# Optimization experiments

Hardware: AMD Instinct MI355X
Metric: run time of the kernel (lower is better)

## Reference

```python
import jax, jax.numpy as jnp
import numpy as np

N = 100000
E = 1600000
IN_DIM = 128
HID = 64
HEADS = 1
NEG_SLOPE = 0.2


def setup_inputs() -> dict:
    key = jax.random.key(0)
    ks = jax.random.split(key, 12)
    x = jax.random.normal(ks[0], (N, IN_DIM), dtype=jnp.float32)
    edge_index = jax.random.randint(ks[1], (2, E), 0, N, dtype=jnp.int64)
    s1 = 1.0 / np.sqrt(IN_DIM)
    s2 = 1.0 / np.sqrt(HEADS * HID)
    return {
        "x": x,
        "edge_index": edge_index,
        # layer 1: in_dim -> heads*hid
        "W1": jax.random.normal(ks[2], (IN_DIM, HEADS * HID), dtype=jnp.float32) * s1,
        "a_src1": jax.random.normal(ks[3], (HEADS, HID), dtype=jnp.float32) * s1,
        "a_dst1": jax.random.normal(ks[4], (HEADS, HID), dtype=jnp.float32) * s1,
        "b1": jnp.zeros((HEADS * HID,), dtype=jnp.float32),
        # layer 2: heads*hid -> hid (1 head)
        "W2": jax.random.normal(ks[5], (HEADS * HID, HID), dtype=jnp.float32) * s2,
        "a_src2": jax.random.normal(ks[6], (1, HID), dtype=jnp.float32) * s2,
        "a_dst2": jax.random.normal(ks[7], (1, HID), dtype=jnp.float32) * s2,
        "b2": jnp.zeros((HID,), dtype=jnp.float32),
        # output head
        "W_out": jax.random.normal(ks[8], (HID, 1), dtype=jnp.float32) * (1.0 / np.sqrt(HID)),
        "b_out": jnp.zeros((1,), dtype=jnp.float32),
    }


def _gat_conv(x, src, dst, W, a_src, a_dst, bias, heads, hid):
    n = x.shape[0]
    h = (x @ W).reshape(n, heads, hid)                      # [N, H, D]
    alpha_s = jnp.einsum("nhd,hd->nh", h, a_src)            # [N, H]
    alpha_d = jnp.einsum("nhd,hd->nh", h, a_dst)
    e = alpha_s[src] + alpha_d[dst]                          # [E, H]
    e = jax.nn.leaky_relu(e, NEG_SLOPE)
    # segment softmax over edges sharing the same destination node
    m = jax.ops.segment_max(e, dst, num_segments=n)          # [N, H]
    ex = jnp.exp(e - m[dst])
    denom = jax.ops.segment_sum(ex, dst, num_segments=n)     # [N, H]
    alpha = ex / denom[dst]                                  # [E, H]
    out = jax.ops.segment_sum(h[src] * alpha[:, :, None], dst, num_segments=n)
    return out.reshape(n, heads * hid) + bias


def reference(x, edge_index, W1, a_src1, a_dst1, b1, W2, a_src2, a_dst2, b2, W_out, b_out):
    n = x.shape[0]
    # PyG GATConv default add_self_loops=True
    loops = jnp.arange(n, dtype=edge_index.dtype)
    src = jnp.concatenate([edge_index[0], loops])
    dst = jnp.concatenate([edge_index[1], loops])
    h = jax.nn.elu(_gat_conv(x, src, dst, W1, a_src1, a_dst1, b1, HEADS, HID))
    h = jax.nn.elu(_gat_conv(h, src, dst, W2, a_src2, a_dst2, b2, 1, HID))
    return (h @ W_out + b_out).squeeze(-1)                   # [N]
```

## Files before the change

kernel.cpp:

```cpp
#include <hip/hip_runtime.h>
#include <hip/hip_fp16.h>
#include <math.h>

#define NEG_SLOPE 0.2f
#define BKT_SHIFT 8
#define BKT_NODES (1 << BKT_SHIFT)
#define BKT_CAP 512
#define BKT_FCAP 6144
#define BKT_SHARD (BKT_FCAP / 4)
#define P1_CHUNK 4096

typedef _Float16 f16x8 __attribute__((ext_vector_type(8)));
typedef float    f32x4 __attribute__((ext_vector_type(4)));
union FU  { uint4 u; f16x8 f; };
union H2U { __half2 h; unsigned u; };

__device__ __forceinline__ float lrelu(float x){ return fmaxf(x, NEG_SLOPE * x); }
__device__ __forceinline__ float elu_fast(float x){
  float t = __expf(fminf(x, 0.f)) - 1.f;
  return x > 0.f ? x : t;
}


__global__ __launch_bounds__(256) void k_p1(const int* __restrict__ src, const int* __restrict__ dst,
                                            int E, int B, int* __restrict__ bktCur,
                                            unsigned* __restrict__ pairs,
                                            const float* __restrict__ W1, const float* __restrict__ W2,
                                            uint4* __restrict__ W1f, uint4* __restrict__ W2f){
  __shared__ int h[BKT_CAP], base[BKT_CAP], cur[BKT_CAP];
  int tid = threadIdx.x;
  if (blockIdx.x == 0){
    for (int idx = tid; idx < 16 * 64; idx += 256){
      int lane = idx & 63, fs = idx >> 6;
      int t = fs >> 2, s = fs & 3;
      int m = lane & 15, quad = lane >> 4;
      f16x8 v;
      #pragma unroll
      for (int j = 0; j < 8; ++j)
        v[j] = (_Float16)W1[(s * 32 + quad * 8 + j) * 64 + t * 16 + m];
      FU fu; fu.f = v;
      W1f[fs * 64 + lane] = fu.u;
    }
    for (int idx = tid; idx < 8 * 64; idx += 256){
      int lane = idx & 63, fs = idx >> 6;
      int t = fs >> 1, s = fs & 1;
      int m = lane & 15, quad = lane >> 4;
      f16x8 v;
      #pragma unroll
      for (int j = 0; j < 8; ++j)
        v[j] = (_Float16)W2[(s * 32 + quad * 8 + j) * 64 + t * 16 + m];
      FU fu; fu.f = v;
      W2f[fs * 64 + lane] = fu.u;
    }
  }
  for (int i = tid; i < BKT_CAP; i += 256){ h[i] = 0; cur[i] = 0; }
  __syncthreads();
  int beg = blockIdx.x * P1_CHUNK;
  int end = min(beg + P1_CHUNK, E);
  int shard = blockIdx.x & 3;
  int m4 = (end - beg) >> 2;
  const int4* d4 = (const int4*)(dst + beg);
  const int4* s4 = (const int4*)(src + beg);
  for (int i = tid; i < m4; i += 256){
    int4 d = d4[i];
    atomicAdd(&h[d.x >> BKT_SHIFT], 1); atomicAdd(&h[d.y >> BKT_SHIFT], 1);
    atomicAdd(&h[d.z >> BKT_SHIFT], 1); atomicAdd(&h[d.w >> BKT_SHIFT], 1);
  }
  for (int i = beg + (m4 << 2) + tid; i < end; i += 256)
    atomicAdd(&h[dst[i] >> BKT_SHIFT], 1);
  __syncthreads();
  for (int i = tid; i < B; i += 256)
    if (h[i]) base[i] = i * BKT_FCAP + shard * BKT_SHARD + atomicAdd(&bktCur[i * 4 + shard], h[i]);
  __syncthreads();
  for (int i = tid; i < m4; i += 256){
    int4 d = d4[i]; int4 s = s4[i];
    int b0 = d.x >> BKT_SHIFT, b1 = d.y >> BKT_SHIFT, b2 = d.z >> BKT_SHIFT, b3 = d.w >> BKT_SHIFT;
    int p0 = base[b0] + atomicAdd(&cur[b0], 1);
    pairs[p0] = ((unsigned)(d.x & (BKT_NODES-1)) << 17) | (unsigned)s.x;
    int p1 = base[b1] + atomicAdd(&cur[b1], 1);
    pairs[p1] = ((unsigned)(d.y & (BKT_NODES-1)) << 17) | (unsigned)s.y;
    int p2 = base[b2] + atomicAdd(&cur[b2], 1);
    pairs[p2] = ((unsigned)(d.z & (BKT_NODES-1)) << 17) | (unsigned)s.z;
    int p3 = base[b3] + atomicAdd(&cur[b3], 1);
    pairs[p3] = ((unsigned)(d.w & (BKT_NODES-1)) << 17) | (unsigned)s.w;
  }
  for (int i = beg + (m4 << 2) + tid; i < end; i += 256){
    int d = dst[i], s = src[i];
    int b = d >> BKT_SHIFT;
    int p = base[b] + atomicAdd(&cur[b], 1);
    pairs[p] = ((unsigned)(d & (BKT_NODES-1)) << 17) | (unsigned)s;
  }
}

__global__ __launch_bounds__(256) void k_p2(const unsigned* __restrict__ pairs,
                                            const int* __restrict__ bktCur,
                                            int N, int2* __restrict__ offs2, int* __restrict__ col){
  __shared__ int sc[BKT_NODES], cu[BKT_NODES];
  int b = blockIdx.x, tid = threadIdx.x;
  int nbase = b << BKT_SHIFT;
  int bs = b * BKT_FCAP;
  sc[tid] = 0;
  __syncthreads();
  #pragma unroll
  for (int s = 0; s < 4; ++s){
    int ss_ = bs + s * BKT_SHARD;
    int se_ = ss_ + bktCur[b * 4 + s];
    for (int i = ss_ + tid; i < se_; i += 256)
      atomicAdd(&sc[pairs[i] >> 17], 1);
  }
  __syncthreads();
  int v = sc[tid];
  for (int o = 1; o < 256; o <<= 1){
    int x = (tid >= o) ? sc[tid - o] : 0;
    __syncthreads();
    sc[tid] += x;
    __syncthreads();
  }
  int ex = sc[tid] - v;
  cu[tid] = bs + ex;
  if (nbase + tid < N) offs2[nbase + tid] = make_int2(bs + ex, bs + ex + v);
  __syncthreads();
  #pragma unroll
  for (int s = 0; s < 4; ++s){
    int ss_ = bs + s * BKT_SHARD;
    int se_ = ss_ + bktCur[b * 4 + s];
    for (int i = ss_ + tid; i < se_; i += 256){
      unsigned pr = pairs[i];
      int p = atomicAdd(&cu[pr >> 17], 1);
      col[p] = (int)(pr & 0x1FFFFu);
    }
  }
}

__global__ __launch_bounds__(256) void k_mgemm1(
    const float* __restrict__ X, const uint4* __restrict__ Wf,
    const float* __restrict__ a_src, const float* __restrict__ a_dst,
    uint2* __restrict__ H, float* __restrict__ as_, float* __restrict__ ad_, int n)
{
  int lane = threadIdx.x & 63, wv = threadIdx.x >> 6;
  int quad = lane >> 4, nn = lane & 15;
  int rowb = blockIdx.x * 64 + wv * 16;
  int row = rowb + nn;
  bool ok = row < n;
  int rowc = ok ? row : n - 1;

  f16x8 af[4][4];
  #pragma unroll
  for (int t = 0; t < 4; ++t)
    #pragma unroll
    for (int s = 0; s < 4; ++s){
      FU fu; fu.u = Wf[(t * 4 + s) * 64 + lane];
      af[t][s] = fu.f;
    }

  const float4* Xr = (const float4*)(X + (size_t)rowc * 128);
  float4 xb[4][2];
  #pragma unroll
  for (int s = 0; s < 4; ++s){
    xb[s][0] = Xr[s * 8 + quad * 2];
    xb[s][1] = Xr[s * 8 + quad * 2 + 1];
  }

  f32x4 acc[4] = {};
  #pragma unroll
  for (int s = 0; s < 4; ++s){
    f16x8 bf;
    bf[0] = (_Float16)xb[s][0].x; bf[1] = (_Float16)xb[s][0].y;
    bf[2] = (_Float16)xb[s][0].z; bf[3] = (_Float16)xb[s][0].w;
    bf[4] = (_Float16)xb[s][1].x; bf[5] = (_Float16)xb[s][1].y;
    bf[6] = (_Float16)xb[s][1].z; bf[7] = (_Float16)xb[s][1].w;
    #pragma unroll
    for (int t = 0; t < 4; ++t)
      acc[t] = __builtin_amdgcn_mfma_f32_16x16x32_f16(af[t][s], bf, acc[t], 0, 0, 0);
  }

  if (ok){
    #pragma unroll
    for (int t = 0; t < 4; ++t){
      H2U p0, p1;
      p0.h = __floats2half2_rn(acc[t][0], acc[t][1]);
      p1.h = __floats2half2_rn(acc[t][2], acc[t][3]);
      H[(size_t)row * 16 + t * 4 + quad] = make_uint2(p0.u, p1.u);
    }
  }
  float sl = 0.f, dl = 0.f;
  #pragma unroll
  for (int t = 0; t < 4; ++t){
    float4 a4 = ((const float4*)a_src)[t * 4 + quad];
    float4 d4 = ((const float4*)a_dst)[t * 4 + quad];
    sl += acc[t][0] * a4.x + acc[t][1] * a4.y + acc[t][2] * a4.z + acc[t][3] * a4.w;
    dl += acc[t][0] * d4.x + acc[t][1] * d4.y + acc[t][2] * d4.z + acc[t][3] * d4.w;
  }
  sl += __shfl_xor(sl, 16, 64); sl += __shfl_xor(sl, 32, 64);
  dl += __shfl_xor(dl, 16, 64); dl += __shfl_xor(dl, 32, 64);
  if (lane < 16 && ok){ as_[row] = sl; ad_[row] = dl; }
}

__global__ __launch_bounds__(256) void k_mgemm2(
    const uint4* __restrict__ Xh, const uint4* __restrict__ Wf,
    const float* __restrict__ a_src, const float* __restrict__ a_dst,
    uint2* __restrict__ H, float* __restrict__ as_, float* __restrict__ ad_, int n)
{
  int lane = threadIdx.x & 63, wv = threadIdx.x >> 6;
  int quad = lane >> 4, nn = lane & 15;
  int rowb = blockIdx.x * 64 + wv * 16;
  int row = rowb + nn;
  bool ok = row < n;
  int rowc = ok ? row : n - 1;

  f16x8 af[4][2];
  #pragma unroll
  for (int t = 0; t < 4; ++t)
    #pragma unroll
    for (int s = 0; s < 2; ++s){
      FU fu; fu.u = Wf[(t * 2 + s) * 64 + lane];
      af[t][s] = fu.f;
    }

  f16x8 bf[2];
  #pragma unroll
  for (int s = 0; s < 2; ++s){
    FU fu; fu.u = Xh[(size_t)rowc * 8 + s * 4 + quad];
    bf[s] = fu.f;
  }

  f32x4 acc[4] = {};
  #pragma unroll
  for (int s = 0; s < 2; ++s)
    #pragma unroll
    for (int t = 0; t < 4; ++t)
      acc[t] = __builtin_amdgcn_mfma_f32_16x16x32_f16(af[t][s], bf[s], acc[t], 0, 0, 0);

  if (ok){
    #pragma unroll
    for (int t = 0; t < 4; ++t){
      H2U p0, p1;
      p0.h = __floats2half2_rn(acc[t][0], acc[t][1]);
      p1.h = __floats2half2_rn(acc[t][2], acc[t][3]);
      H[(size_t)row * 16 + t * 4 + quad] = make_uint2(p0.u, p1.u);
    }
  }
  float sl = 0.f, dl = 0.f;
  #pragma unroll
  for (int t = 0; t < 4; ++t){
    float4 a4 = ((const float4*)a_src)[t * 4 + quad];
    float4 d4 = ((const float4*)a_dst)[t * 4 + quad];
    sl += acc[t][0] * a4.x + acc[t][1] * a4.y + acc[t][2] * a4.z + acc[t][3] * a4.w;
    dl += acc[t][0] * d4.x + acc[t][1] * d4.y + acc[t][2] * d4.z + acc[t][3] * d4.w;
  }
  sl += __shfl_xor(sl, 16, 64); sl += __shfl_xor(sl, 32, 64);
  dl += __shfl_xor(dl, 16, 64); dl += __shfl_xor(dl, 32, 64);
  if (lane < 16 && ok){ as_[row] = sl; ad_[row] = dl; }
}

#define FMA8(e, hv) { const __half2* hp = (const __half2*)&(hv);               \
  a[0]=fmaf(e, __half2float(hp[0].x), a[0]); a[1]=fmaf(e, __half2float(hp[0].y), a[1]); \
  a[2]=fmaf(e, __half2float(hp[1].x), a[2]); a[3]=fmaf(e, __half2float(hp[1].y), a[3]); \
  a[4]=fmaf(e, __half2float(hp[2].x), a[4]); a[5]=fmaf(e, __half2float(hp[2].y), a[5]); \
  a[6]=fmaf(e, __half2float(hp[3].x), a[6]); a[7]=fmaf(e, __half2float(hp[3].y), a[7]); }

__device__ __forceinline__ void agg_core(
    const int2* __restrict__ offs2, const int* __restrict__ col,
    const uint4* __restrict__ H4, const float* __restrict__ as_, const float* __restrict__ ad_,
    int node, int c8, float& denom, float a[8])
{
  int2 be2 = offs2[node];
  int beg = be2.x, d = be2.y - be2.x;
  int maxd = d;
  maxd = max(maxd, __shfl_xor(maxd, 8, 64));
  maxd = max(maxd, __shfl_xor(maxd, 16, 64));
  maxd = max(maxd, __shfl_xor(maxd, 32, 64));
  float adv = ad_[node];
  float exs = __expf(lrelu(as_[node] + adv));
  uint4 hself = H4[(size_t)node * 8 + c8];
  denom = exs;
  { const __half2* hp = (const __half2*)&hself;
    #pragma unroll
    for (int i = 0; i < 4; ++i){
      a[2*i]   = exs * __half2float(hp[i].x);
      a[2*i+1] = exs * __half2float(hp[i].y);
    } }
  for (int j = 0; j < maxd; j += 4){
    int ss[4]; float asv[4]; uint4 hv[4];
    #pragma unroll
    for (int u = 0; u < 4; ++u) ss[u] = (j + u < d) ? col[beg + j + u] : 0;
    #pragma unroll
    for (int u = 0; u < 4; ++u) asv[u] = as_[ss[u]];
    #pragma unroll
    for (int u = 0; u < 4; ++u) hv[u] = H4[(size_t)ss[u] * 8 + c8];
    #pragma unroll
    for (int u = 0; u < 4; ++u){
      float e = (j + u < d) ? __expf(lrelu(asv[u] + adv)) : 0.f;
      denom += e;
      FMA8(e, hv[u])
    }
  }
}

__global__ __launch_bounds__(256) void k_agg1(
    const int2* __restrict__ offs2, const int* __restrict__ col,
    const uint4* __restrict__ H4, const float* __restrict__ as_, const float* __restrict__ ad_,
    const float* __restrict__ bias, uint4* __restrict__ outH, int n)
{
  int lane = threadIdx.x & 63, w = threadIdx.x >> 6;
  int m = lane >> 3, c8 = lane & 7;
  float4 b0 = *(const float4*)&bias[8 * c8];
  float4 b1 = *(const float4*)&bias[8 * c8 + 4];
  float bb[8] = {b0.x, b0.y, b0.z, b0.w, b1.x, b1.y, b1.z, b1.w};
  #pragma unroll
  for (int g = 0; g < 2; ++g){
    int node0 = blockIdx.x * 64 + g * 32 + w * 8 + m;
    bool ok = node0 < n;
    int node = ok ? node0 : n - 1;
    float denom; float a[8];
    agg_core(offs2, col, H4, as_, ad_, node, c8, denom, a);
    float inv = 1.f / denom;
    unsigned oh[4];
    #pragma unroll
    for (int i = 0; i < 4; ++i){
      float v0 = elu_fast(fmaf(a[2*i],   inv, bb[2*i]));
      float v1 = elu_fast(fmaf(a[2*i+1], inv, bb[2*i+1]));
      __half2 h = __floats2half2_rn(v0, v1);
      oh[i] = *(unsigned*)&h;
    }
    if (ok){
      uint4 ov; ov.x = oh[0]; ov.y = oh[1]; ov.z = oh[2]; ov.w = oh[3];
      outH[(size_t)node * 8 + c8] = ov;
    }
  }
}

__global__ __launch_bounds__(256) void k_agg2(
    const int2* __restrict__ offs2, const int* __restrict__ col,
    const uint4* __restrict__ H4, const float* __restrict__ as_, const float* __restrict__ ad_,
    const float* __restrict__ bias, const float* __restrict__ Wout, const float* __restrict__ bout,
    float* __restrict__ out, int n)
{
  int lane = threadIdx.x & 63, w = threadIdx.x >> 6;
  int m = lane >> 3, c8 = lane & 7;
  float4 b0 = *(const float4*)&bias[8 * c8];
  float4 b1 = *(const float4*)&bias[8 * c8 + 4];
  float4 w0 = *(const float4*)&Wout[8 * c8];
  float4 w1 = *(const float4*)&Wout[8 * c8 + 4];
  float bb[8] = {b0.x, b0.y, b0.z, b0.w, b1.x, b1.y, b1.z, b1.w};
  float ww[8] = {w0.x, w0.y, w0.z, w0.w, w1.x, w1.y, w1.z, w1.w};
  #pragma unroll
  for (int g = 0; g < 2; ++g){
    int node0 = blockIdx.x * 64 + g * 32 + w * 8 + m;
    bool ok = node0 < n;
    int node = ok ? node0 : n - 1;
    float denom; float a[8];
    agg_core(offs2, col, H4, as_, ad_, node, c8, denom, a);
    float inv = 1.f / denom;
    float p = 0.f;
    #pragma unroll
    for (int i = 0; i < 8; ++i)
      p += elu_fast(fmaf(a[i], inv, bb[i])) * ww[i];
    p += __shfl_xor(p, 1, 64); p += __shfl_xor(p, 2, 64); p += __shfl_xor(p, 4, 64);
    if (c8 == 0 && ok) out[node] = p + bout[0];
  }
}

extern "C" void kernel_launch(void* const* d_in, const int* in_sizes, int n_in,
                              void* d_out, int out_size, void* d_ws, size_t ws_size,
                              hipStream_t stream)
{
  const float* x    = (const float*)d_in[0];
  const int*   ei   = (const int*)d_in[1];
  const float* W1   = (const float*)d_in[2];
  const float* as1w = (const float*)d_in[3];
  const float* ad1w = (const float*)d_in[4];
  const float* b1   = (const float*)d_in[5];
  const float* W2   = (const float*)d_in[6];
  const float* as2w = (const float*)d_in[7];
  const float* ad2w = (const float*)d_in[8];
  const float* b2   = (const float*)d_in[9];
  const float* Wout = (const float*)d_in[10];
  const float* bout = (const float*)d_in[11];
  float* out = (float*)d_out;

  const int N = in_sizes[0] / 128;
  const int E = in_sizes[1] / 2;
  const int* srcA = ei;
  const int* dstA = ei + E;
  const int B = (N + BKT_NODES - 1) >> BKT_SHIFT;

  char* p = (char*)d_ws;
  auto alloc = [&](size_t bytes){ char* r = p; p += (bytes + 255) & ~255ull; return r; };
  int*   bktCur = (int*)alloc(BKT_CAP * 4 * 4);
  int2*  offs2  = (int2*)alloc((size_t)N * 8);
  int*   col    = (int*)alloc((size_t)B * BKT_FCAP * 4);
  float* vas1 = (float*)alloc((size_t)N * 4);
  float* vad1 = (float*)alloc((size_t)N * 4);
  float* vas2 = (float*)alloc((size_t)N * 4);
  float* vad2 = (float*)alloc((size_t)N * 4);
  uint4* w1f  = (uint4*)alloc(16 * 64 * 16);
  uint4* w2f  = (uint4*)alloc(8 * 64 * 16);
  uint2* h1   = (uint2*)alloc((size_t)N * 64 * 2);
  uint2* h1e  = (uint2*)alloc((size_t)N * 64 * 2);
  unsigned* pairs = (unsigned*)h1;
  uint2* h2   = h1;

  hipMemsetAsync(bktCur, 0, BKT_CAP * 4 * 4, stream);

  int nchunk = (E + P1_CHUNK - 1) / P1_CHUNK;
  k_p1<<<nchunk, 256, 0, stream>>>(srcA, dstA, E, B, bktCur, pairs, W1, W2, w1f, w2f);
  k_p2<<<B, 256, 0, stream>>>(pairs, bktCur, N, offs2, col);

  int gblocks = (N + 63) / 64;
  int ablocks = (N + 63) / 64;
  k_mgemm1<<<gblocks, 256, 0, stream>>>(x, w1f, as1w, ad1w, h1, vas1, vad1, N);
  k_agg1  <<<ablocks, 256, 0, stream>>>(offs2, col, (const uint4*)h1, vas1, vad1, b1, (uint4*)h1e, N);
  k_mgemm2<<<gblocks, 256, 0, stream>>>((const uint4*)h1e, w2f, as2w, ad2w, h2, vas2, vad2, N);
  k_agg2  <<<ablocks, 256, 0, stream>>>(offs2, col, (const uint4*)h2, vas2, vad2, b2, Wout, bout, out, N);
}
```

Baseline: 258.4 us.

## Fuse layer-2 GEMM into layer-1 aggregation via shared-memory staging

The layer-1 aggregation kernel now writes its ELU'd fp16 output into shared memory, and two waves per block then run the layer-2 MFMA GEMM and the attention-logit dot products directly on it. This removes the separate k_mgemm2 launch and the global round trip of the intermediate h1e activations. Aggregation blocks now cover 32 nodes each instead of looping over 64, so twice as many blocks launch. The costs are an added __syncthreads and two of four waves sitting idle during the GEMM phase. h2 gets its own buffer instead of aliasing h1.

```diff
diff --git a/kernel.cpp b/kernel.cpp
--- a/kernel.cpp
+++ b/kernel.cpp
@@ -196,63 +196,6 @@
   if (lane < 16 && ok){ as_[row] = sl; ad_[row] = dl; }
 }
 
-__global__ __launch_bounds__(256) void k_mgemm2(
-    const uint4* __restrict__ Xh, const uint4* __restrict__ Wf,
-    const float* __restrict__ a_src, const float* __restrict__ a_dst,
-    uint2* __restrict__ H, float* __restrict__ as_, float* __restrict__ ad_, int n)
-{
-  int lane = threadIdx.x & 63, wv = threadIdx.x >> 6;
-  int quad = lane >> 4, nn = lane & 15;
-  int rowb = blockIdx.x * 64 + wv * 16;
-  int row = rowb + nn;
-  bool ok = row < n;
-  int rowc = ok ? row : n - 1;
-
-  f16x8 af[4][2];
-  #pragma unroll
-  for (int t = 0; t < 4; ++t)
-    #pragma unroll
-    for (int s = 0; s < 2; ++s){
-      FU fu; fu.u = Wf[(t * 2 + s) * 64 + lane];
-      af[t][s] = fu.f;
-    }
-
-  f16x8 bf[2];
-  #pragma unroll
-  for (int s = 0; s < 2; ++s){
-    FU fu; fu.u = Xh[(size_t)rowc * 8 + s * 4 + quad];
-    bf[s] = fu.f;
-  }
-
-  f32x4 acc[4] = {};
-  #pragma unroll
-  for (int s = 0; s < 2; ++s)
-    #pragma unroll
-    for (int t = 0; t < 4; ++t)
-      acc[t] = __builtin_amdgcn_mfma_f32_16x16x32_f16(af[t][s], bf[s], acc[t], 0, 0, 0);
-
-  if (ok){
-    #pragma unroll
-    for (int t = 0; t < 4; ++t){
-      H2U p0, p1;
-      p0.h = __floats2half2_rn(acc[t][0], acc[t][1]);
-      p1.h = __floats2half2_rn(acc[t][2], acc[t][3]);
-      H[(size_t)row * 16 + t * 4 + quad] = make_uint2(p0.u, p1.u);
-    }
-  }
-  float sl = 0.f, dl = 0.f;
-  #pragma unroll
-  for (int t = 0; t < 4; ++t){
-    float4 a4 = ((const float4*)a_src)[t * 4 + quad];
-    float4 d4 = ((const float4*)a_dst)[t * 4 + quad];
-    sl += acc[t][0] * a4.x + acc[t][1] * a4.y + acc[t][2] * a4.z + acc[t][3] * a4.w;
-    dl += acc[t][0] * d4.x + acc[t][1] * d4.y + acc[t][2] * d4.z + acc[t][3] * d4.w;
-  }
-  sl += __shfl_xor(sl, 16, 64); sl += __shfl_xor(sl, 32, 64);
-  dl += __shfl_xor(dl, 16, 64); dl += __shfl_xor(dl, 32, 64);
-  if (lane < 16 && ok){ as_[row] = sl; ad_[row] = dl; }
-}
-
 #define FMA8(e, hv) { const __half2* hp = (const __half2*)&(hv);               \
   a[0]=fmaf(e, __half2float(hp[0].x), a[0]); a[1]=fmaf(e, __half2float(hp[0].y), a[1]); \
   a[2]=fmaf(e, __half2float(hp[1].x), a[2]); a[3]=fmaf(e, __half2float(hp[1].y), a[3]); \
@@ -297,36 +240,84 @@
   }
 }
 
-__global__ __launch_bounds__(256) void k_agg1(
+__global__ __launch_bounds__(256) void k_agg1f(
     const int2* __restrict__ offs2, const int* __restrict__ col,
     const uint4* __restrict__ H4, const float* __restrict__ as_, const float* __restrict__ ad_,
-    const float* __restrict__ bias, uint4* __restrict__ outH, int n)
+    const float* __restrict__ bias, const uint4* __restrict__ W2f,
+    const float* __restrict__ a_src2, const float* __restrict__ a_dst2,
+    uint2* __restrict__ H2out, float* __restrict__ as2_, float* __restrict__ ad2_, int n)
 {
+  __shared__ unsigned uhl[32][36];
   int lane = threadIdx.x & 63, w = threadIdx.x >> 6;
   int m = lane >> 3, c8 = lane & 7;
+  int node0 = blockIdx.x * 32 + w * 8 + m;
+  bool ok = node0 < n;
+  int node = ok ? node0 : n - 1;
+  float denom; float a[8];
+  agg_core(offs2, col, H4, as_, ad_, node, c8, denom, a);
+  float inv = 1.f / denom;
   float4 b0 = *(const float4*)&bias[8 * c8];
   float4 b1 = *(const float4*)&bias[8 * c8 + 4];
   float bb[8] = {b0.x, b0.y, b0.z, b0.w, b1.x, b1.y, b1.z, b1.w};
-  #pragma unroll
-  for (int g = 0; g < 2; ++g){
-    int node0 = blockIdx.x * 64 + g * 32 + w * 8 + m;
-    bool ok = node0 < n;
-    int node = ok ? node0 : n - 1;
-    float denom; float a[8];
-    agg_core(offs2, col, H4, as_, ad_, node, c8, denom, a);
-    float inv = 1.f / denom;
-    unsigned oh[4];
-    #pragma unroll
-    for (int i = 0; i < 4; ++i){
-      float v0 = elu_fast(fmaf(a[2*i],   inv, bb[2*i]));
-      float v1 = elu_fast(fmaf(a[2*i+1], inv, bb[2*i+1]));
-      __half2 h = __floats2half2_rn(v0, v1);
-      oh[i] = *(unsigned*)&h;
-    }
-    if (ok){
-      uint4 ov; ov.x = oh[0]; ov.y = oh[1]; ov.z = oh[2]; ov.w = oh[3];
-      outH[(size_t)node * 8 + c8] = ov;
-    }
+  int ln = w * 8 + m;
+  #pragma unroll
+  for (int i = 0; i < 4; ++i){
+    float v0 = elu_fast(fmaf(a[2*i],   inv, bb[2*i]));
+    float v1 = elu_fast(fmaf(a[2*i+1], inv, bb[2*i+1]));
+    __half2 h = __floats2half2_rn(v0, v1);
+    uhl[ln][c8 * 4 + i] = *(unsigned*)&h;
+  }
+  __syncthreads();
+
+  if (w < 2){
+    int quad = lane >> 4, nn = lane & 15;
+    int lrow = w * 16 + nn;
+    int row = blockIdx.x * 32 + lrow;
+    bool ok2 = row < n;
+
+    f16x8 af[4][2];
+    #pragma unroll
+    for (int t = 0; t < 4; ++t)
+      #pragma unroll
+      for (int s = 0; s < 2; ++s){
+        FU fu; fu.u = W2f[(t * 2 + s) * 64 + lane];
+        af[t][s] = fu.f;
+      }
+
+    f16x8 bf[2];
+    #pragma unroll
+    for (int s = 0; s < 2; ++s){
+      FU fu; fu.u = ((const uint4*)&uhl[lrow][0])[s * 4 + quad];
+      bf[s] = fu.f;
+    }
+
+    f32x4 acc[4] = {};
+    #pragma unroll
+    for (int s = 0; s < 2; ++s)
+      #pragma unroll
+      for (int t = 0; t < 4; ++t)
+        acc[t] = __builtin_amdgcn_mfma_f32_16x16x32_f16(af[t][s], bf[s], acc[t], 0, 0, 0);
+
+    if (ok2){
+      #pragma unroll
+      for (int t = 0; t < 4; ++t){
+        H2U p0, p1;
+        p0.h = __floats2half2_rn(acc[t][0], acc[t][1]);
+        p1.h = __floats2half2_rn(acc[t][2], acc[t][3]);
+        H2out[(size_t)row * 16 + t * 4 + quad] = make_uint2(p0.u, p1.u);
+      }
+    }
+    float sl = 0.f, dl = 0.f;
+    #pragma unroll
+    for (int t = 0; t < 4; ++t){
+      float4 a4 = ((const float4*)a_src2)[t * 4 + quad];
+      float4 d4 = ((const float4*)a_dst2)[t * 4 + quad];
+      sl += acc[t][0] * a4.x + acc[t][1] * a4.y + acc[t][2] * a4.z + acc[t][3] * a4.w;
+      dl += acc[t][0] * d4.x + acc[t][1] * d4.y + acc[t][2] * d4.z + acc[t][3] * d4.w;
+    }
+    sl += __shfl_xor(sl, 16, 64); sl += __shfl_xor(sl, 32, 64);
+    dl += __shfl_xor(dl, 16, 64); dl += __shfl_xor(dl, 32, 64);
+    if (lane < 16 && ok2){ as2_[row] = sl; ad2_[row] = dl; }
   }
 }
 
@@ -338,27 +329,24 @@
 {
   int lane = threadIdx.x & 63, w = threadIdx.x >> 6;
   int m = lane >> 3, c8 = lane & 7;
+  int node0 = blockIdx.x * 32 + w * 8 + m;
+  bool ok = node0 < n;
+  int node = ok ? node0 : n - 1;
+  float denom; float a[8];
+  agg_core(offs2, col, H4, as_, ad_, node, c8, denom, a);
+  float inv = 1.f / denom;
   float4 b0 = *(const float4*)&bias[8 * c8];
   float4 b1 = *(const float4*)&bias[8 * c8 + 4];
   float4 w0 = *(const float4*)&Wout[8 * c8];
   float4 w1 = *(const float4*)&Wout[8 * c8 + 4];
   float bb[8] = {b0.x, b0.y, b0.z, b0.w, b1.x, b1.y, b1.z, b1.w};
   float ww[8] = {w0.x, w0.y, w0.z, w0.w, w1.x, w1.y, w1.z, w1.w};
-  #pragma unroll
-  for (int g = 0; g < 2; ++g){
-    int node0 = blockIdx.x * 64 + g * 32 + w * 8 + m;
-    bool ok = node0 < n;
-    int node = ok ? node0 : n - 1;
-    float denom; float a[8];
-    agg_core(offs2, col, H4, as_, ad_, node, c8, denom, a);
-    float inv = 1.f / denom;
-    float p = 0.f;
-    #pragma unroll
-    for (int i = 0; i < 8; ++i)
-      p += elu_fast(fmaf(a[i], inv, bb[i])) * ww[i];
-    p += __shfl_xor(p, 1, 64); p += __shfl_xor(p, 2, 64); p += __shfl_xor(p, 4, 64);
-    if (c8 == 0 && ok) out[node] = p + bout[0];
-  }
+  float p = 0.f;
+  #pragma unroll
+  for (int i = 0; i < 8; ++i)
+    p += elu_fast(fmaf(a[i], inv, bb[i])) * ww[i];
+  p += __shfl_xor(p, 1, 64); p += __shfl_xor(p, 2, 64); p += __shfl_xor(p, 4, 64);
+  if (c8 == 0 && ok) out[node] = p + bout[0];
 }
 
 extern "C" void kernel_launch(void* const* d_in, const int* in_sizes, int n_in,
@@ -397,9 +385,8 @@
   uint4* w1f  = (uint4*)alloc(16 * 64 * 16);
   uint4* w2f  = (uint4*)alloc(8 * 64 * 16);
   uint2* h1   = (uint2*)alloc((size_t)N * 64 * 2);
-  uint2* h1e  = (uint2*)alloc((size_t)N * 64 * 2);
+  uint2* h2   = (uint2*)alloc((size_t)N * 64 * 2);
   unsigned* pairs = (unsigned*)h1;
-  uint2* h2   = h1;
 
   hipMemsetAsync(bktCur, 0, BKT_CAP * 4 * 4, stream);
 
@@ -408,9 +395,9 @@
   k_p2<<<B, 256, 0, stream>>>(pairs, bktCur, N, offs2, col);
 
   int gblocks = (N + 63) / 64;
-  int ablocks = (N + 63) / 64;
+  int ablocks = (N + 31) / 32;
   k_mgemm1<<<gblocks, 256, 0, stream>>>(x, w1f, as1w, ad1w, h1, vas1, vad1, N);
-  k_agg1  <<<ablocks, 256, 0, stream>>>(offs2, col, (const uint4*)h1, vas1, vad1, b1, (uint4*)h1e, N);
-  k_mgemm2<<<gblocks, 256, 0, stream>>>((const uint4*)h1e, w2f, as2w, ad2w, h2, vas2, vad2, N);
+  k_agg1f <<<ablocks, 256, 0, stream>>>(offs2, col, (const uint4*)h1, vas1, vad1, b1,
+                                        w2f, as2w, ad2w, h2, vas2, vad2, N);
   k_agg2  <<<ablocks, 256, 0, stream>>>(offs2, col, (const uint4*)h2, vas2, vad2, b2, Wout, bout, out, N);
 }
```

After: 245.3 us. -5.1%, faster.
